# Optimization experiments

Hardware: AMD Instinct MI355X
Metric: run time of the kernel (lower is better)

Reference implementation:

```python
import jax, jax.numpy as jnp
import numpy as np

N = 100000      # nodes
E = 1600000     # message-passing edges
P = 1000000     # prediction edges
DIN = 128       # node_in_channels
H = 128         # hidden_channels
DOUT = 64       # out_channels (node embedding)
EIN = 32        # edge_in_channels
EPS = 1e-5


def setup_inputs() -> dict:
    key = jax.random.key(0)
    ks = iter(jax.random.split(key, 48))
    nk = lambda: next(ks)
    rn = lambda shape: jax.random.normal(nk(), shape, dtype=jnp.float32)
    glorot = lambda shape: rn(shape) * (1.0 / np.sqrt(shape[-1]))
    inp = {
        "x": rn((N, DIN)),
        "edge_index": jax.random.randint(nk(), (2, E), 0, N),
        "pred_edge_index": jax.random.randint(nk(), (2, P), 0, N),
        "edge_features": rn((P, EIN)),
        # SAGEConv layer 1: lin_l (aggregated, with bias), lin_r (root, no bias)
        "sage1_Wl": glorot((H, DIN)), "sage1_bl": jnp.zeros((H,), jnp.float32), "sage1_Wr": glorot((H, DIN)),
        "bn1_g": jnp.ones((H,), jnp.float32), "bn1_b": jnp.zeros((H,), jnp.float32),
        "bn1_m": rn((H,)) * 0.1, "bn1_v": jnp.ones((H,), jnp.float32),
        # SAGEConv layer 2
        "sage2_Wl": glorot((DOUT, H)), "sage2_bl": jnp.zeros((DOUT,), jnp.float32), "sage2_Wr": glorot((DOUT, H)),
        # edge MLP: Linear(EIN, H//2) -> BN -> ReLU -> Linear(H//2, H//4)
        "edge_W1": glorot((H // 2, EIN)), "edge_b1": jnp.zeros((H // 2,), jnp.float32),
        "ebn_g": jnp.ones((H // 2,), jnp.float32), "ebn_b": jnp.zeros((H // 2,), jnp.float32),
        "ebn_m": rn((H // 2,)) * 0.1, "ebn_v": jnp.ones((H // 2,), jnp.float32),
        "edge_W2": glorot((H // 4, H // 2)), "edge_b2": jnp.zeros((H // 4,), jnp.float32),
        # predictor: Linear(2*DOUT+H//4, H) -> BN -> ReLU -> Linear(H, H//2) -> BN -> ReLU -> Linear(H//2, 1)
        "p_W1": glorot((H, 2 * DOUT + H // 4)), "p_b1": jnp.zeros((H,), jnp.float32),
        "pbn1_g": jnp.ones((H,), jnp.float32), "pbn1_b": jnp.zeros((H,), jnp.float32),
        "pbn1_m": rn((H,)) * 0.1, "pbn1_v": jnp.ones((H,), jnp.float32),
        "p_W2": glorot((H // 2, H)), "p_b2": jnp.zeros((H // 2,), jnp.float32),
        "pbn2_g": jnp.ones((H // 2,), jnp.float32), "pbn2_b": jnp.zeros((H // 2,), jnp.float32),
        "pbn2_m": rn((H // 2,)) * 0.1, "pbn2_v": jnp.ones((H // 2,), jnp.float32),
        "p_W3": glorot((1, H // 2)), "p_b3": jnp.zeros((1,), jnp.float32),
    }
    return inp


def _bn(h, g, b, m, v):
    # eval-mode BatchNorm1d with running stats
    return (h - m) * (g / jnp.sqrt(v + EPS)) + b


def _sage(h, src, dst, Wl, bl, Wr):
    # PyG SAGEConv (mean aggr): lin_l(mean of h[src] at dst) + lin_r(h)
    msg = jax.ops.segment_sum(h[src], dst, num_segments=N)        # [N, d]
    cnt = jax.ops.segment_sum(jnp.ones((src.shape[0],), h.dtype), dst, num_segments=N)
    agg = msg / jnp.maximum(cnt, 1.0)[:, None]
    return agg @ Wl.T + bl + h @ Wr.T


def reference(x, edge_index, pred_edge_index, edge_features,
              sage1_Wl, sage1_bl, sage1_Wr, bn1_g, bn1_b, bn1_m, bn1_v,
              sage2_Wl, sage2_bl, sage2_Wr,
              edge_W1, edge_b1, ebn_g, ebn_b, ebn_m, ebn_v, edge_W2, edge_b2,
              p_W1, p_b1, pbn1_g, pbn1_b, pbn1_m, pbn1_v,
              p_W2, p_b2, pbn2_g, pbn2_b, pbn2_m, pbn2_v, p_W3, p_b3):
    src, dst = edge_index[0], edge_index[1]
    # GraphSAGE encoder (eval mode: dropout off, BN running stats)
    h = _sage(x, src, dst, sage1_Wl, sage1_bl, sage1_Wr)
    h = jax.nn.relu(_bn(h, bn1_g, bn1_b, bn1_m, bn1_v))
    z = _sage(h, src, dst, sage2_Wl, sage2_bl, sage2_Wr)          # [N, DOUT]
    # edge-pair gather + concat
    combined = jnp.concatenate([z[pred_edge_index[0]], z[pred_edge_index[1]]], axis=-1)  # [P, 2*DOUT]
    # edge feature MLP
    e = edge_features @ edge_W1.T + edge_b1
    e = jax.nn.relu(_bn(e, ebn_g, ebn_b, ebn_m, ebn_v))
    e = e @ edge_W2.T + edge_b2                                   # [P, H//4]
    combined = jnp.concatenate([combined, e], axis=-1)            # [P, 2*DOUT + H//4]
    # predictor MLP
    u = combined @ p_W1.T + p_b1
    u = jax.nn.relu(_bn(u, pbn1_g, pbn1_b, pbn1_m, pbn1_v))
    u = u @ p_W2.T + p_b2
    u = jax.nn.relu(_bn(u, pbn2_g, pbn2_b, pbn2_m, pbn2_v))
    out = u @ p_W3.T + p_b3                                       # [P, 1]
    return out[:, 0]
```

## Files before the change

### kernel.cpp

```cpp
#include <hip/hip_runtime.h>

#define Nn 100000
#define Ee 1600000
#define Pp 1000000
#define EPSf 1e-5f

typedef _Float16 f16x8 __attribute__((ext_vector_type(8)));
typedef _Float16 f16x4 __attribute__((ext_vector_type(4)));
typedef _Float16 f16x2 __attribute__((ext_vector_type(2)));
typedef float f32x4 __attribute__((ext_vector_type(4)));

__device__ __forceinline__ float4 ld4(const float* p) { return *(const float4*)p; }

#define oW1l 0
#define oW1r 16384
#define oW2l 32768
#define oW2r 40960
#define oW1a 49152
#define oW1b 57344
#define oW1c 65536
#define oWe1 69632
#define oWe2 71680
#define oWp2 73728
#define W16_TOTAL 81920

#define BN_TOTAL 608

__global__ __launch_bounds__(256) void prep_kernel(
    const float* __restrict__ x,
    const float* __restrict__ s1Wl, const float* __restrict__ s1Wr,
    const float* __restrict__ s2Wl, const float* __restrict__ s2Wr,
    const float* __restrict__ pW1,  const float* __restrict__ eW1,
    const float* __restrict__ eW2,  const float* __restrict__ pW2,
    const float* __restrict__ eb1,
    const float* __restrict__ ebng, const float* __restrict__ ebnb,
    const float* __restrict__ ebnm, const float* __restrict__ ebnv,
    const float* __restrict__ eb2,
    const float* __restrict__ pb1,
    const float* __restrict__ p1g, const float* __restrict__ p1b,
    const float* __restrict__ p1m, const float* __restrict__ p1v,
    const float* __restrict__ pb2,
    const float* __restrict__ p2g, const float* __restrict__ p2b,
    const float* __restrict__ p2m, const float* __restrict__ p2v,
    const float* __restrict__ pW3,
    _Float16* __restrict__ w16, float* __restrict__ bnA,
    _Float16* __restrict__ x16) {
    int tid = blockIdx.x * 256 + threadIdx.x;
    if (tid < W16_TOTAL) {
        float v;
        if (tid < 16384)      v = s1Wl[tid];
        else if (tid < 32768) v = s1Wr[tid - 16384];
        else if (tid < 40960) v = s2Wl[tid - 32768];
        else if (tid < 49152) v = s2Wr[tid - 40960];
        else if (tid < 57344) { int l = tid - 49152; v = pW1[(l >> 6) * 160 + (l & 63)]; }
        else if (tid < 65536) { int l = tid - 57344; v = pW1[(l >> 6) * 160 + 64 + (l & 63)]; }
        else if (tid < 69632) { int l = tid - 65536; v = pW1[(l >> 5) * 160 + 128 + (l & 31)]; }
        else if (tid < 71680) v = eW1[tid - 69632];
        else if (tid < 73728) v = eW2[tid - 71680];
        else                  v = pW2[tid - 73728];
        w16[tid] = (_Float16)v;
    } else if (tid < W16_TOTAL + BN_TOTAL) {
        int b = tid - W16_TOTAL;
        float v;
        if (b < 64)       v = ebng[b] * rsqrtf(ebnv[b] + EPSf);
        else if (b < 128) { int c = b - 64;  float s = ebng[c] * rsqrtf(ebnv[c] + EPSf);
                            v = (eb1[c] - ebnm[c]) * s + ebnb[c]; }
        else if (b < 256) { int c = b - 128; v = p1g[c] * rsqrtf(p1v[c] + EPSf); }
        else if (b < 384) { int c = b - 256; float s = p1g[c] * rsqrtf(p1v[c] + EPSf);
                            v = (pb1[c] - p1m[c]) * s + p1b[c]; }
        else if (b < 448) { int c = b - 384; v = p2g[c] * rsqrtf(p2v[c] + EPSf); }
        else if (b < 512) { int c = b - 448; float s = p2g[c] * rsqrtf(p2v[c] + EPSf);
                            v = (pb2[c] - p2m[c]) * s + p2b[c]; }
        else if (b < 544) v = eb2[b - 512];
        else              v = pW3[b - 544];
        bnA[b] = v;
    }
    int stride = gridDim.x * 256;
    const int NV = Nn * 128 / 4;
    for (int i = tid; i < NV; i += stride) {
        float4 v = ((const float4*)x)[i];
        f16x4 h = {(_Float16)v.x, (_Float16)v.y, (_Float16)v.z, (_Float16)v.w};
        ((f16x4*)x16)[i] = h;
    }
}

__global__ __launch_bounds__(256) void hist_kernel(const int* __restrict__ dst,
                                                   unsigned* __restrict__ deg) {
    int i = blockIdx.x * 256 + threadIdx.x;
    if (i < Ee) atomicAdd(&deg[dst[i]], 1u);
}

__global__ __launch_bounds__(1024) void scanA_kernel(const unsigned* __restrict__ deg,
                                                     unsigned* __restrict__ escan,
                                                     unsigned* __restrict__ bsum) {
    __shared__ unsigned s[1024];
    int t = threadIdx.x;
    int gid = blockIdx.x * 1024 + t;
    unsigned v = (gid < Nn) ? deg[gid] : 0u;
    s[t] = v;
    __syncthreads();
    for (int off = 1; off < 1024; off <<= 1) {
        unsigned u = (t >= off) ? s[t - off] : 0u;
        __syncthreads();
        s[t] += u;
        __syncthreads();
    }
    if (gid < Nn) escan[gid] = s[t] - v;
    if (t == 1023) bsum[blockIdx.x] = s[1023];
}

__global__ __launch_bounds__(128) void scanB_kernel(const unsigned* __restrict__ bsum,
                                                    unsigned* __restrict__ boff,
                                                    int nblk) {
    __shared__ unsigned s[128];
    int t = threadIdx.x;
    unsigned v = (t < nblk) ? bsum[t] : 0u;
    s[t] = v;
    __syncthreads();
    for (int off = 1; off < 128; off <<= 1) {
        unsigned u = (t >= off) ? s[t - off] : 0u;
        __syncthreads();
        s[t] += u;
        __syncthreads();
    }
    if (t < nblk) boff[t] = s[t] - v;
}

__global__ __launch_bounds__(1024) void scanC_kernel(const unsigned* __restrict__ escan,
                                                     const unsigned* __restrict__ boff,
                                                     int* __restrict__ rowptr,
                                                     int* __restrict__ cursor) {
    int t = threadIdx.x;
    int gid = blockIdx.x * 1024 + t;
    if (gid < Nn) {
        int v = (int)(escan[gid] + boff[blockIdx.x]);
        rowptr[gid] = v;
        cursor[gid] = v;
    }
    if (gid == 0) rowptr[Nn] = Ee;
}

__global__ __launch_bounds__(256) void scatter_kernel(const int* __restrict__ src,
                                                      const int* __restrict__ dst,
                                                      int* __restrict__ cursor,
                                                      int* __restrict__ elist) {
    int i = blockIdx.x * 256 + threadIdx.x;
    if (i < Ee) {
        int p = atomicAdd(&cursor[dst[i]], 1);
        elist[p] = src[i];
    }
}

template<int W>
__global__ __launch_bounds__(256, 8) void aggregate16_kernel(
    const _Float16* __restrict__ feat,
    const int* __restrict__ rowptr,
    const int* __restrict__ elist,
    _Float16* __restrict__ outp) {
    int node = (blockIdx.x * 256 + threadIdx.x) >> 6;
    int lane = threadIdx.x & 63;
    if (node >= Nn) return;
    constexpr int SEGS = W / 8;
    constexpr int RPI  = 64 / SEGS;
    constexpr int B    = (RPI >= 8) ? 2 : 4;
    const int r = lane / SEGS, c = lane % SEGS;
    int beg = rowptr[node], end = rowptr[node + 1];
    int n = end - beg;
    float acc[8];
#pragma unroll
    for (int k = 0; k < 8; ++k) acc[k] = 0.f;
    for (int c0 = 0; c0 < n; c0 += 64) {
        int m = min(64, n - c0);
        int se = (lane < m) ? elist[beg + c0 + lane] : 0;
        int iters = (m + RPI - 1) / RPI;
        int ff = m / RPI;
        int i = 0;
        for (; i + B <= ff; i += B) {
            int sA[B]; f16x8 vA[B];
#pragma unroll
            for (int k = 0; k < B; ++k) sA[k] = __shfl(se, (i + k) * RPI + r);
#pragma unroll
            for (int k = 0; k < B; ++k)
                vA[k] = *(const f16x8*)(feat + (size_t)sA[k] * W + c * 8);
#pragma unroll
            for (int k = 0; k < B; ++k)
#pragma unroll
                for (int q = 0; q < 8; ++q) acc[q] += (float)vA[k][q];
        }
        for (; i < iters; ++i) {
            int j = i * RPI + r;
            int s = __shfl(se, j);
            if (j < m) {
                f16x8 v = *(const f16x8*)(feat + (size_t)s * W + c * 8);
#pragma unroll
                for (int q = 0; q < 8; ++q) acc[q] += (float)v[q];
            }
        }
    }
#pragma unroll
    for (int k = 0; k < 8; ++k) {
#pragma unroll
        for (int off = SEGS; off < 64; off <<= 1)
            acc[k] += __shfl_xor(acc[k], off);
    }
    if (r == 0) {
        float inv = 1.0f / fmaxf((float)n, 1.0f);
        f16x8 o;
#pragma unroll
        for (int k = 0; k < 8; ++k) o[k] = (_Float16)(acc[k] * inv);
        *(f16x8*)(outp + (size_t)node * W + c * 8) = o;
    }
}

__global__ __launch_bounds__(256) void dense1_kernel(
    const _Float16* __restrict__ A1, const _Float16* __restrict__ A2,
    const _Float16* __restrict__ W1, const _Float16* __restrict__ W2,
    const float* __restrict__ lb,
    const float* __restrict__ bng, const float* __restrict__ bnb,
    const float* __restrict__ bnm, const float* __restrict__ bnv,
    _Float16* __restrict__ out) {
    const int t = threadIdx.x;
    const int w = t >> 6, lane = t & 63;
    const int lrow = lane & 15, lq = lane >> 4;
    const int row0 = blockIdx.x * 64 + w * 16;
    const int ld = min(row0 + lrow, Nn - 1);

    f16x8 a1[4], a2[4];
#pragma unroll
    for (int i = 0; i < 4; ++i) {
        a1[i] = *(const f16x8*)(A1 + (size_t)ld * 128 + i * 32 + lq * 8);
        a2[i] = *(const f16x8*)(A2 + (size_t)ld * 128 + i * 32 + lq * 8);
    }
#pragma unroll
    for (int nt = 0; nt < 8; ++nt) {
        const _Float16* w1r = W1 + (size_t)(nt * 16 + lrow) * 128;
        const _Float16* w2r = W2 + (size_t)(nt * 16 + lrow) * 128;
        f32x4 c = {0.f, 0.f, 0.f, 0.f};
#pragma unroll
        for (int i = 0; i < 4; ++i) {
            c = __builtin_amdgcn_mfma_f32_16x16x32_f16(a1[i], *(const f16x8*)(w1r + i * 32 + lq * 8), c, 0, 0, 0);
            c = __builtin_amdgcn_mfma_f32_16x16x32_f16(a2[i], *(const f16x8*)(w2r + i * 32 + lq * 8), c, 0, 0, 0);
        }
        int cc = nt * 16 + lrow;
        float s = bng[cc] * rsqrtf(bnv[cc] + EPSf);
        float h = (lb[cc] - bnm[cc]) * s + bnb[cc];
#pragma unroll
        for (int r = 0; r < 4; ++r) {
            int gr = row0 + lq * 4 + r;
            if (gr < Nn)
                out[(size_t)gr * 128 + cc] = (_Float16)fmaxf(c[r] * s + h, 0.f);
        }
    }
}

__global__ __launch_bounds__(256) void gemmY_kernel(
    const _Float16* __restrict__ A, const _Float16* __restrict__ W,
    _Float16* __restrict__ out) {
    const int t = threadIdx.x;
    const int w = t >> 6, lane = t & 63;
    const int lrow = lane & 15, lq = lane >> 4;
    const int row0 = blockIdx.x * 64 + w * 16;
    const int ld = min(row0 + lrow, Nn - 1);
    f16x8 a[4];
#pragma unroll
    for (int i = 0; i < 4; ++i)
        a[i] = *(const f16x8*)(A + (size_t)ld * 128 + i * 32 + lq * 8);
#pragma unroll
    for (int nt = 0; nt < 4; ++nt) {
        const _Float16* wr = W + (size_t)(nt * 16 + lrow) * 128;
        f32x4 c = {0.f, 0.f, 0.f, 0.f};
#pragma unroll
        for (int i = 0; i < 4; ++i)
            c = __builtin_amdgcn_mfma_f32_16x16x32_f16(a[i], *(const f16x8*)(wr + i * 32 + lq * 8), c, 0, 0, 0);
        int cc = nt * 16 + lrow;
#pragma unroll
        for (int r = 0; r < 4; ++r) {
            int gr = row0 + lq * 4 + r;
            if (gr < Nn) out[(size_t)gr * 64 + cc] = (_Float16)c[r];
        }
    }
}

__global__ __launch_bounds__(256) void dense2b_kernel(
    const _Float16* __restrict__ aggY, const _Float16* __restrict__ A2,
    const _Float16* __restrict__ W2, const float* __restrict__ lb,
    _Float16* __restrict__ out) {
    const int t = threadIdx.x;
    const int w = t >> 6, lane = t & 63;
    const int lrow = lane & 15, lq = lane >> 4;
    const int row0 = blockIdx.x * 64 + w * 16;
    const int ld = min(row0 + lrow, Nn - 1);
    f16x8 a[4];
#pragma unroll
    for (int i = 0; i < 4; ++i)
        a[i] = *(const f16x8*)(A2 + (size_t)ld * 128 + i * 32 + lq * 8);
#pragma unroll
    for (int nt = 0; nt < 4; ++nt) {
        const _Float16* wr = W2 + (size_t)(nt * 16 + lrow) * 128;
        f32x4 c = {0.f, 0.f, 0.f, 0.f};
#pragma unroll
        for (int i = 0; i < 4; ++i)
            c = __builtin_amdgcn_mfma_f32_16x16x32_f16(a[i], *(const f16x8*)(wr + i * 32 + lq * 8), c, 0, 0, 0);
        int cc = nt * 16 + lrow;
        float b = lb[cc];
#pragma unroll
        for (int r = 0; r < 4; ++r) {
            int gr = row0 + lq * 4 + r;
            if (gr < Nn) {
                float g = (float)aggY[(size_t)gr * 64 + cc];
                out[(size_t)gr * 64 + cc] = (_Float16)(c[r] + g + b);
            }
        }
    }
}

__global__ __launch_bounds__(256) void emlp_kernel(
    const float* __restrict__ ef,
    const _Float16* __restrict__ w16,
    const float* __restrict__ bnA,
    _Float16* __restrict__ e2out) {
    __shared__ __align__(16) _Float16 E1[64 * 72];
    const int t = threadIdx.x;
    const int lane = t & 63, w = t >> 6;
    const int lrow = lane & 15, lq = lane >> 4;
    const int e0 = blockIdx.x * 64 + w * 16;
    const int erow = w * 16 + lrow;

    const float* src = ef + (size_t)(e0 + lrow) * 32 + lq * 8;
    float4 f0 = ld4(src), f1 = ld4(src + 4);
    f16x8 bf = {(_Float16)f0.x, (_Float16)f0.y, (_Float16)f0.z, (_Float16)f0.w,
                (_Float16)f1.x, (_Float16)f1.y, (_Float16)f1.z, (_Float16)f1.w};

#pragma unroll
    for (int nt = 0; nt < 4; ++nt) {
        f16x8 wf = *(const f16x8*)(w16 + oWe1 + (nt * 16 + lrow) * 32 + lq * 8);
        f32x4 c = {0.f, 0.f, 0.f, 0.f};
        c = __builtin_amdgcn_mfma_f32_16x16x32_f16(wf, bf, c, 0, 0, 0);
        int cb = nt * 16 + lq * 4;
        float4 s = *(const float4*)(bnA + cb);
        float4 h = *(const float4*)(bnA + 64 + cb);
        f16x4 o;
        o[0] = (_Float16)fmaxf(c[0] * s.x + h.x, 0.f);
        o[1] = (_Float16)fmaxf(c[1] * s.y + h.y, 0.f);
        o[2] = (_Float16)fmaxf(c[2] * s.z + h.z, 0.f);
        o[3] = (_Float16)fmaxf(c[3] * s.w + h.w, 0.f);
        *(f16x4*)(E1 + erow * 72 + cb) = o;
    }
    f16x8 a0 = *(const f16x8*)(E1 + erow * 72 + lq * 8);
    f16x8 a1 = *(const f16x8*)(E1 + erow * 72 + 32 + lq * 8);
#pragma unroll
    for (int nt = 0; nt < 2; ++nt) {
        f16x8 b0 = *(const f16x8*)(w16 + oWe2 + (nt * 16 + lrow) * 64 + lq * 8);
        f16x8 b1 = *(const f16x8*)(w16 + oWe2 + (nt * 16 + lrow) * 64 + 32 + lq * 8);
        f32x4 c = {0.f, 0.f, 0.f, 0.f};
        c = __builtin_amdgcn_mfma_f32_16x16x32_f16(b0, a0, c, 0, 0, 0);
        c = __builtin_amdgcn_mfma_f32_16x16x32_f16(b1, a1, c, 0, 0, 0);
        int cb = nt * 16 + lq * 4;
        float4 bias = *(const float4*)(bnA + 512 + cb);
        f16x4 o;
        o[0] = (_Float16)(c[0] + bias.x);
        o[1] = (_Float16)(c[1] + bias.y);
        o[2] = (_Float16)(c[2] + bias.z);
        o[3] = (_Float16)(c[3] + bias.w);
        *(f16x4*)(e2out + (size_t)(e0 + lrow) * 32 + cb) = o;
    }
}

#define EPB 256
#define NT  ((Pp + EPB - 1) / EPB)
#define EGRID 256

#define oL_W1a 0
#define oL_W1b 18432
#define oL_W1c 36864
#define oL_Wp2 47104
#define oL_BN  64512
#define oL_ZU  66304
#define SMEM_BYTES 135936

__global__ __launch_bounds__(1024, 4) void edge_kernel(
    const int* __restrict__ pe,
    const _Float16* __restrict__ e2,
    const _Float16* __restrict__ z,
    const _Float16* __restrict__ w16,
    const float* __restrict__ bnA,
    const float* __restrict__ pb3,
    float* __restrict__ out) {
    __shared__ __align__(16) unsigned char smem[SMEM_BYTES];
    _Float16* LW1a = (_Float16*)(smem + oL_W1a);
    _Float16* LW1b = (_Float16*)(smem + oL_W1b);
    _Float16* LW1c = (_Float16*)(smem + oL_W1c);
    _Float16* LWp2 = (_Float16*)(smem + oL_Wp2);
    float*    LBN  = (float*)(smem + oL_BN);
    _Float16* ZU   = (_Float16*)(smem + oL_ZU);

    const float* bn2s = LBN;        const float* bn2h = LBN + 128;
    const float* bn3s = LBN + 256;  const float* bn3h = LBN + 320;
    const float* wp3g = LBN + 384;

    const int t = threadIdx.x;
    const int lane = t & 63;
    const int w = t >> 6;
    const int m0 = w * 16;
    const int lrow = lane & 15;
    const int lq = lane >> 4;
    const float pb3v = pb3[0];

    auto load_idx = [&](int tl, int& ia, int& ib) {
        int e = min(tl * EPB + m0 + lrow, Pp - 1);
        ia = pe[e];
        ib = pe[Pp + e];
    };
    auto gather = [&](int tl, int ia, int ib, f16x8* F) {
        F[0] = *(const f16x8*)(z + (size_t)ia * 64 + lq * 8);
        F[1] = *(const f16x8*)(z + (size_t)ia * 64 + 32 + lq * 8);
        F[2] = *(const f16x8*)(z + (size_t)ib * 64 + lq * 8);
        F[3] = *(const f16x8*)(z + (size_t)ib * 64 + 32 + lq * 8);
        int e = min(tl * EPB + m0 + lrow, Pp - 1);
        F[4] = *(const f16x8*)(e2 + (size_t)e * 32 + lq * 8);
    };

    int tile = blockIdx.x;
    int ia1, ib1;
    {
        int ia0, ib0;
        load_idx(tile, ia0, ib0);
        load_idx(tile + EGRID, ia1, ib1);
        f16x8 F[5];
        gather(tile, ia0, ib0, F);

        { int r = t >> 3, s = t & 7;
          *(f16x8*)(LW1a + r * 72 + s * 8) = *(const f16x8*)(w16 + oW1a + r * 64 + s * 8);
          *(f16x8*)(LW1b + r * 72 + s * 8) = *(const f16x8*)(w16 + oW1b + r * 64 + s * 8); }
        if (t < 512) { int r = t >> 2, s = t & 3;
          *(f16x8*)(LW1c + r * 40 + s * 8) = *(const f16x8*)(w16 + oW1c + r * 32 + s * 8); }
        { int r = t >> 4, s = t & 15;
          *(f16x8*)(LWp2 + r * 136 + s * 8) = *(const f16x8*)(w16 + oWp2 + r * 128 + s * 8); }
        if (t < 384) LBN[t] = bnA[128 + t];
        else if (t < 448) LBN[t] = bnA[544 + (t - 384)];
        __syncthreads();

        const int erow = m0 + lrow;
        const int zr = erow * 136;
        for (; tile < NT; tile += EGRID) {
            f16x8 G[5];
            gather(tile + EGRID, ia1, ib1, G);
            int ia2, ib2;
            load_idx(tile + 2 * EGRID, ia2, ib2);

            const bool act = (tile * EPB + m0) < Pp;
            if (act) {
                __builtin_amdgcn_s_setprio(1);
#pragma unroll
                for (int nt = 0; nt < 8; ++nt) {
                    const _Float16* wa = LW1a + (nt * 16 + lrow) * 72;
                    const _Float16* wb = LW1b + (nt * 16 + lrow) * 72;
                    const _Float16* wc = LW1c + (nt * 16 + lrow) * 40;
                    f32x4 c = {0.f, 0.f, 0.f, 0.f};
                    c = __builtin_amdgcn_mfma_f32_16x16x32_f16(*(const f16x8*)(wa + lq * 8),      F[0], c, 0, 0, 0);
                    c = __builtin_amdgcn_mfma_f32_16x16x32_f16(*(const f16x8*)(wa + 32 + lq * 8), F[1], c, 0, 0, 0);
                    c = __builtin_amdgcn_mfma_f32_16x16x32_f16(*(const f16x8*)(wb + lq * 8),      F[2], c, 0, 0, 0);
                    c = __builtin_amdgcn_mfma_f32_16x16x32_f16(*(const f16x8*)(wb + 32 + lq * 8), F[3], c, 0, 0, 0);
                    c = __builtin_amdgcn_mfma_f32_16x16x32_f16(*(const f16x8*)(wc + lq * 8),      F[4], c, 0, 0, 0);
                    int cb = nt * 16 + lq * 4;
                    float4 s = *(const float4*)(bn2s + cb);
                    float4 h = *(const float4*)(bn2h + cb);
                    f16x4 o;
                    o[0] = (_Float16)fmaxf(c[0] * s.x + h.x, 0.f);
                    o[1] = (_Float16)fmaxf(c[1] * s.y + h.y, 0.f);
                    o[2] = (_Float16)fmaxf(c[2] * s.z + h.z, 0.f);
                    o[3] = (_Float16)fmaxf(c[3] * s.w + h.w, 0.f);
                    *(f16x4*)(ZU + zr + cb) = o;
                }
                __builtin_amdgcn_s_setprio(0);
                {
                    f16x8 a0 = *(const f16x8*)(ZU + zr + 0  + lq * 8);
                    f16x8 a1 = *(const f16x8*)(ZU + zr + 32 + lq * 8);
                    f16x8 a2 = *(const f16x8*)(ZU + zr + 64 + lq * 8);
                    f16x8 a3 = *(const f16x8*)(ZU + zr + 96 + lq * 8);
                    float acc = 0.f;
                    __builtin_amdgcn_s_setprio(1);
#pragma unroll
                    for (int nt = 0; nt < 4; ++nt) {
                        const _Float16* wr = LWp2 + (nt * 16 + lrow) * 136 + lq * 8;
                        f32x4 c = {0.f, 0.f, 0.f, 0.f};
                        c = __builtin_amdgcn_mfma_f32_16x16x32_f16(*(const f16x8*)(wr + 0),  a0, c, 0, 0, 0);
                        c = __builtin_amdgcn_mfma_f32_16x16x32_f16(*(const f16x8*)(wr + 32), a1, c, 0, 0, 0);
                        c = __builtin_amdgcn_mfma_f32_16x16x32_f16(*(const f16x8*)(wr + 64), a2, c, 0, 0, 0);
                        c = __builtin_amdgcn_mfma_f32_16x16x32_f16(*(const f16x8*)(wr + 96), a3, c, 0, 0, 0);
                        int cb = nt * 16 + lq * 4;
                        float4 s  = *(const float4*)(bn3s + cb);
                        float4 h  = *(const float4*)(bn3h + cb);
                        float4 w3 = *(const float4*)(wp3g + cb);
                        acc += fmaxf(c[0] * s.x + h.x, 0.f) * w3.x;
                        acc += fmaxf(c[1] * s.y + h.y, 0.f) * w3.y;
                        acc += fmaxf(c[2] * s.z + h.z, 0.f) * w3.z;
                        acc += fmaxf(c[3] * s.w + h.w, 0.f) * w3.w;
                    }
                    __builtin_amdgcn_s_setprio(0);
                    acc += __shfl_xor(acc, 16);
                    acc += __shfl_xor(acc, 32);
                    if (lane < 16) out[tile * EPB + m0 + lane] = acc + pb3v;
                }
            }
#pragma unroll
            for (int i = 0; i < 5; ++i) F[i] = G[i];
            ia1 = ia2; ib1 = ib2;
        }
    }
}

extern "C" void kernel_launch(void* const* d_in, const int* in_sizes, int n_in,
                              void* d_out, int out_size, void* d_ws, size_t ws_size,
                              hipStream_t stream) {
    const float* x    = (const float*)d_in[0];
    const int*   eidx = (const int*)d_in[1];
    const int*   pe   = (const int*)d_in[2];
    const float* ef   = (const float*)d_in[3];
    const float* s1Wl = (const float*)d_in[4];
    const float* s1bl = (const float*)d_in[5];
    const float* s1Wr = (const float*)d_in[6];
    const float* bn1g = (const float*)d_in[7];
    const float* bn1b = (const float*)d_in[8];
    const float* bn1m = (const float*)d_in[9];
    const float* bn1v = (const float*)d_in[10];
    const float* s2Wl = (const float*)d_in[11];
    const float* s2bl = (const float*)d_in[12];
    const float* s2Wr = (const float*)d_in[13];
    const float* eW1  = (const float*)d_in[14];
    const float* eb1  = (const float*)d_in[15];
    const float* ebng = (const float*)d_in[16];
    const float* ebnb = (const float*)d_in[17];
    const float* ebnm = (const float*)d_in[18];
    const float* ebnv = (const float*)d_in[19];
    const float* eW2  = (const float*)d_in[20];
    const float* eb2  = (const float*)d_in[21];
    const float* pW1  = (const float*)d_in[22];
    const float* pb1  = (const float*)d_in[23];
    const float* p1g  = (const float*)d_in[24];
    const float* p1b  = (const float*)d_in[25];
    const float* p1m  = (const float*)d_in[26];
    const float* p1v  = (const float*)d_in[27];
    const float* pW2  = (const float*)d_in[28];
    const float* pb2  = (const float*)d_in[29];
    const float* p2g  = (const float*)d_in[30];
    const float* p2b  = (const float*)d_in[31];
    const float* p2m  = (const float*)d_in[32];
    const float* p2v  = (const float*)d_in[33];
    const float* pW3  = (const float*)d_in[34];
    const float* pb3  = (const float*)d_in[35];
    float* out = (float*)d_out;

    char* wk = (char*)d_ws;
    auto carve = [&](size_t bytes) {
        char* p = wk;
        wk += (bytes + 255) & ~(size_t)255;
        return p;
    };
    unsigned*  deg    = (unsigned*)carve((size_t)Nn * 4);
    int*       rowptr = (int*)carve((size_t)(Nn + 1) * 4);
    int*       cursor = (int*)carve((size_t)Nn * 4);
    int*       elist  = (int*)carve((size_t)Ee * 4);
    unsigned*  escan  = (unsigned*)carve((size_t)Nn * 4);
    unsigned*  bsum   = (unsigned*)carve(128 * 4);
    unsigned*  boff   = (unsigned*)carve(128 * 4);
    _Float16*  w16    = (_Float16*)carve((size_t)W16_TOTAL * 2);
    float*     bnA    = (float*)carve((size_t)BN_TOTAL * 4);
    _Float16*  bufX   = (_Float16*)carve((size_t)Nn * 128 * 2);
    _Float16*  bufA   = (_Float16*)carve((size_t)Nn * 128 * 2);
    _Float16*  bufH   = (_Float16*)carve((size_t)Nn * 128 * 2);
    _Float16*  e2buf  = (_Float16*)carve((size_t)Pp * 32 * 2);
    _Float16*  bufY   = bufX;
    _Float16*  bufZ   = bufX + (size_t)Nn * 64;
    _Float16*  bufAy  = bufA;

    const int* e_src = eidx;
    const int* e_dst = eidx + Ee;
    const int SBLK = (Nn + 1023) / 1024;

    hipMemsetAsync(deg, 0, (size_t)Nn * 4, stream);
    prep_kernel<<<800, 256, 0, stream>>>(x, s1Wl, s1Wr, s2Wl, s2Wr, pW1, eW1, eW2, pW2,
                                         eb1, ebng, ebnb, ebnm, ebnv, eb2,
                                         pb1, p1g, p1b, p1m, p1v,
                                         pb2, p2g, p2b, p2m, p2v, pW3,
                                         w16, bnA, bufX);
    emlp_kernel<<<Pp / 64, 256, 0, stream>>>(ef, w16, bnA, e2buf);

    hist_kernel<<<(Ee + 255) / 256, 256, 0, stream>>>(e_dst, deg);
    scanA_kernel<<<SBLK, 1024, 0, stream>>>(deg, escan, bsum);
    scanB_kernel<<<1, 128, 0, stream>>>(bsum, boff, SBLK);
    scanC_kernel<<<SBLK, 1024, 0, stream>>>(escan, boff, rowptr, cursor);
    scatter_kernel<<<(Ee + 255) / 256, 256, 0, stream>>>(e_src, e_dst, cursor, elist);

    aggregate16_kernel<128><<<Nn / 4, 256, 0, stream>>>(bufX, rowptr, elist, bufA);
    dense1_kernel<<<(Nn + 63) / 64, 256, 0, stream>>>(
        bufA, bufX, w16 + oW1l, w16 + oW1r, s1bl, bn1g, bn1b, bn1m, bn1v, bufH);

    gemmY_kernel<<<(Nn + 63) / 64, 256, 0, stream>>>(bufH, w16 + oW2l, bufY);
    aggregate16_kernel<64><<<Nn / 4, 256, 0, stream>>>(bufY, rowptr, elist, bufAy);
    dense2b_kernel<<<(Nn + 63) / 64, 256, 0, stream>>>(
        bufAy, bufH, w16 + oW2r, s2bl, bufZ);

    edge_kernel<<<EGRID, 1024, 0, stream>>>(pe, e2buf, bufZ, w16, bnA, pb3, out);
}
```

Before: 808.7 us.

## Build CSR via bucketed staging and simplify aggregation gather loop

Replaces the histogram-plus-atomic-scatter CSR build with a bucket pass. Edges are binned by destination block (256 nodes) into 8 per-group staging regions with packed src/local-dst words. A per-bucket kernel then places them into elist using shared-memory cursors. This aims to turn scattered global writes and atomics into more local ones. The trade-off is extra global atomics on the bucket counters, and a fixed staging capacity per bucket that could overflow on skewed degree distributions. The aggregation inner loop also drops the manual batched gather in favour of a simple loop with unroll 2.

```diff
diff --git a/kernel.cpp b/kernel.cpp
--- a/kernel.cpp
+++ b/kernel.cpp
@@ -25,6 +25,10 @@
 #define W16_TOTAL 81920
 
 #define BN_TOTAL 608
+
+#define NBUC 391
+#define SCAP 1024
+#define SGROUPS 8
 
 __global__ __launch_bounds__(256) void prep_kernel(
     const float* __restrict__ x,
@@ -84,10 +88,21 @@
     }
 }
 
-__global__ __launch_bounds__(256) void hist_kernel(const int* __restrict__ dst,
-                                                   unsigned* __restrict__ deg) {
-    int i = blockIdx.x * 256 + threadIdx.x;
-    if (i < Ee) atomicAdd(&deg[dst[i]], 1u);
+__global__ __launch_bounds__(256) void bucket_kernel(
+    const int* __restrict__ src, const int* __restrict__ dst,
+    unsigned* __restrict__ deg,
+    unsigned* __restrict__ stage, unsigned* __restrict__ gcur) {
+    const int g = blockIdx.x & 7;
+    const unsigned gb = g * NBUC;
+    int stride = gridDim.x * 256;
+    for (int i = blockIdx.x * 256 + threadIdx.x; i < Ee; i += stride) {
+        int d = dst[i];
+        int s = src[i];
+        atomicAdd(&deg[d], 1u);
+        int b = d >> 8;
+        unsigned p = atomicAdd(&gcur[gb + b], 1u);
+        stage[((size_t)(gb + b)) * SCAP + p] = ((unsigned)s << 8) | (unsigned)(d & 255);
+    }
 }
 
 __global__ __launch_bounds__(1024) void scanA_kernel(const unsigned* __restrict__ deg,
@@ -128,26 +143,37 @@
 
 __global__ __launch_bounds__(1024) void scanC_kernel(const unsigned* __restrict__ escan,
                                                      const unsigned* __restrict__ boff,
-                                                     int* __restrict__ rowptr,
-                                                     int* __restrict__ cursor) {
+                                                     int* __restrict__ rowptr) {
     int t = threadIdx.x;
     int gid = blockIdx.x * 1024 + t;
-    if (gid < Nn) {
-        int v = (int)(escan[gid] + boff[blockIdx.x]);
-        rowptr[gid] = v;
-        cursor[gid] = v;
-    }
+    if (gid < Nn) rowptr[gid] = (int)(escan[gid] + boff[blockIdx.x]);
     if (gid == 0) rowptr[Nn] = Ee;
 }
 
-__global__ __launch_bounds__(256) void scatter_kernel(const int* __restrict__ src,
-                                                      const int* __restrict__ dst,
-                                                      int* __restrict__ cursor,
-                                                      int* __restrict__ elist) {
-    int i = blockIdx.x * 256 + threadIdx.x;
-    if (i < Ee) {
-        int p = atomicAdd(&cursor[dst[i]], 1);
-        elist[p] = src[i];
+__global__ __launch_bounds__(256) void partC_kernel(
+    const unsigned* __restrict__ stage, const unsigned* __restrict__ gcur,
+    const int* __restrict__ rowptr, int* __restrict__ elist) {
+    __shared__ int lbase[256];
+    __shared__ unsigned lcur[256];
+    const int b = blockIdx.x;
+    const int n0 = b << 8;
+    {
+        int node = n0 + threadIdx.x;
+        lbase[threadIdx.x] = (node < Nn) ? rowptr[node] : 0;
+        lcur[threadIdx.x] = 0u;
+    }
+    __syncthreads();
+#pragma unroll 1
+    for (int g = 0; g < SGROUPS; ++g) {
+        unsigned cnt = gcur[g * NBUC + b];
+        const unsigned* sp = stage + ((size_t)(g * NBUC + b)) * SCAP;
+        for (unsigned i = threadIdx.x; i < cnt; i += 256) {
+            unsigned v = sp[i];
+            int lidx = v & 255;
+            int s = (int)(v >> 8);
+            unsigned p = atomicAdd(&lcur[lidx], 1u);
+            elist[lbase[lidx] + p] = s;
+        }
     }
 }
 
@@ -162,7 +188,6 @@
     if (node >= Nn) return;
     constexpr int SEGS = W / 8;
     constexpr int RPI  = 64 / SEGS;
-    constexpr int B    = (RPI >= 8) ? 2 : 4;
     const int r = lane / SEGS, c = lane % SEGS;
     int beg = rowptr[node], end = rowptr[node + 1];
     int n = end - beg;
@@ -173,27 +198,14 @@
         int m = min(64, n - c0);
         int se = (lane < m) ? elist[beg + c0 + lane] : 0;
         int iters = (m + RPI - 1) / RPI;
-        int ff = m / RPI;
-        int i = 0;
-        for (; i + B <= ff; i += B) {
-            int sA[B]; f16x8 vA[B];
-#pragma unroll
-            for (int k = 0; k < B; ++k) sA[k] = __shfl(se, (i + k) * RPI + r);
-#pragma unroll
-            for (int k = 0; k < B; ++k)
-                vA[k] = *(const f16x8*)(feat + (size_t)sA[k] * W + c * 8);
-#pragma unroll
-            for (int k = 0; k < B; ++k)
-#pragma unroll
-                for (int q = 0; q < 8; ++q) acc[q] += (float)vA[k][q];
-        }
-        for (; i < iters; ++i) {
+#pragma unroll 2
+        for (int i = 0; i < iters; ++i) {
             int j = i * RPI + r;
             int s = __shfl(se, j);
             if (j < m) {
                 f16x8 v = *(const f16x8*)(feat + (size_t)s * W + c * 8);
 #pragma unroll
-                for (int q = 0; q < 8; ++q) acc[q] += (float)v[q];
+                for (int k = 0; k < 8; ++k) acc[k] += (float)v[k];
             }
         }
     }
@@ -558,8 +570,8 @@
         return p;
     };
     unsigned*  deg    = (unsigned*)carve((size_t)Nn * 4);
+    unsigned*  gcur   = (unsigned*)carve((size_t)SGROUPS * NBUC * 4);
     int*       rowptr = (int*)carve((size_t)(Nn + 1) * 4);
-    int*       cursor = (int*)carve((size_t)Nn * 4);
     int*       elist  = (int*)carve((size_t)Ee * 4);
     unsigned*  escan  = (unsigned*)carve((size_t)Nn * 4);
     unsigned*  bsum   = (unsigned*)carve(128 * 4);
@@ -573,12 +585,15 @@
     _Float16*  bufY   = bufX;
     _Float16*  bufZ   = bufX + (size_t)Nn * 64;
     _Float16*  bufAy  = bufA;
+    unsigned*  stage  = (unsigned*)bufH;
 
     const int* e_src = eidx;
     const int* e_dst = eidx + Ee;
     const int SBLK = (Nn + 1023) / 1024;
 
-    hipMemsetAsync(deg, 0, (size_t)Nn * 4, stream);
+    size_t degBytes = ((size_t)Nn * 4 + 255) & ~(size_t)255;
+    hipMemsetAsync(deg, 0, degBytes + (size_t)SGROUPS * NBUC * 4, stream);
+
     prep_kernel<<<800, 256, 0, stream>>>(x, s1Wl, s1Wr, s2Wl, s2Wr, pW1, eW1, eW2, pW2,
                                          eb1, ebng, ebnb, ebnm, ebnv, eb2,
                                          pb1, p1g, p1b, p1m, p1v,
@@ -586,11 +601,11 @@
                                          w16, bnA, bufX);
     emlp_kernel<<<Pp / 64, 256, 0, stream>>>(ef, w16, bnA, e2buf);
 
-    hist_kernel<<<(Ee + 255) / 256, 256, 0, stream>>>(e_dst, deg);
+    bucket_kernel<<<512, 256, 0, stream>>>(e_src, e_dst, deg, stage, gcur);
     scanA_kernel<<<SBLK, 1024, 0, stream>>>(deg, escan, bsum);
     scanB_kernel<<<1, 128, 0, stream>>>(bsum, boff, SBLK);
-    scanC_kernel<<<SBLK, 1024, 0, stream>>>(escan, boff, rowptr, cursor);
-    scatter_kernel<<<(Ee + 255) / 256, 256, 0, stream>>>(e_src, e_dst, cursor, elist);
+    scanC_kernel<<<SBLK, 1024, 0, stream>>>(escan, boff, rowptr);
+    partC_kernel<<<NBUC, 256, 0, stream>>>(stage, gcur, rowptr, elist);
 
     aggregate16_kernel<128><<<Nn / 4, 256, 0, stream>>>(bufX, rowptr, elist, bufA);
     dense1_kernel<<<(Nn + 63) / 64, 256, 0, stream>>>(
```

Result: faster. 784.2 us (-3.0%).
